# Kernel tuning notes

Hardware: AMD Instinct MI355X
Metric: run time of the kernel (lower is better)

The kernel has to match this reference:

```python
import jax, jax.numpy as jnp
import numpy as np

EPS = 1e-8  # torch cosine_similarity default eps


def compute_similarity(x, k, dilation=1):
    # x: [B, C, H, W]; returns [B, k*k-1, H, W] cosine similarity of each
    # pixel's channel vector vs its k x k neighborhood (center excluded).
    B, C, H, W = x.shape
    pad = (k // 2) * dilation
    # im2col: [B, C*k*k, H, W], channels ordered (C, kh, kw)
    patches = jax.lax.conv_general_dilated_patches(
        x, (k, k), (1, 1), padding=[(pad, pad), (pad, pad)],
        rhs_dilation=(dilation, dilation))
    patches = patches.reshape(B, C, k * k, H, W)
    center = patches[:, :, k * k // 2]                      # [B, C, H, W]
    dot = jnp.einsum('bchw,bcphw->bphw', center, patches)   # [B, k*k, H, W]
    n_center = jnp.sqrt(jnp.sum(center * center, axis=1))   # [B, H, W]
    n_patch = jnp.sqrt(jnp.sum(patches * patches, axis=1))  # [B, k*k, H, W]
    sim = dot / jnp.maximum(n_center[:, None] * n_patch, EPS)
    # drop the center (self-similarity == 1)
    c = k * k // 2
    return jnp.concatenate([sim[:, :c], sim[:, c + 1:]], axis=1)


def setup_inputs() -> dict:
    key = jax.random.key(0)
    x = jax.random.normal(key, (2, 128, 96, 96), dtype=jnp.float32)
    return {
        'x': x,
        'edge_threshold1': jnp.float32(0.3),
        'edge_threshold2': jnp.float32(0.3),
    }


def reference(x, edge_threshold1, edge_threshold2):
    LARGE_K, SMALL_K, DIL = 9, 5, 1
    large_sim = compute_similarity(x, LARGE_K, DIL)            # [B, 80, H, W]
    large_mask = (large_sim < edge_threshold1).astype(jnp.float32)
    large_mask = jnp.sqrt(jnp.sum(large_mask * large_mask, axis=1, keepdims=True))  # L2 norm over offsets
    x_mask = large_mask * x + x
    small_sim = compute_similarity(x_mask, SMALL_K, DIL)       # [B, 24, H, W]
    small_mask = (small_sim < edge_threshold2).astype(jnp.float32)
    small_mask = jnp.sqrt(jnp.sum(small_mask * small_mask, axis=1, keepdims=True))
    edge_map = x * small_mask + x
    return edge_map
```

## Files before the change

kernel.cpp:

```cpp
#include <hip/hip_runtime.h>

#define BN   2
#define CN   128
#define HN   96
#define WN   96
#define HW   (HN * WN)
#define NPIX (BN * HW)
#define NP4  (NPIX / 4)
#define NTOT (BN * CN * HW)
#define NMAP 13
#define EPSV 1e-8f

constexpr int ODY[12] = {0, 0, 1, 1, 1, 1, 1, 2, 2, 2, 2, 2};
constexpr int ODX[12] = {1, 2, -2, -1, 0, 1, 2, -2, -1, 0, 1, 2};

template<int CPC>
__global__ void __launch_bounds__(64) k_partial(const float* __restrict__ x,
                                                float* __restrict__ P) {
    int p4 = blockIdx.x * blockDim.x + threadIdx.x;
    int chunk = blockIdx.y;
    int nch = gridDim.y;
    int pix = p4 * 4;
    int b = pix / HW;
    int hw = pix - b * HW;
    int h = hw / WN;
    int w = hw - h * WN;
    const float* xb = x + ((size_t)b * CN + (size_t)chunk * CPC) * HW + h * WN + w;

    float acc[NMAP][4];
#pragma unroll
    for (int m = 0; m < NMAP; ++m)
#pragma unroll
        for (int i = 0; i < 4; ++i) acc[m][i] = 0.f;

    for (int cc = 0; cc < CPC; ++cc) {
        const float* cp = xb + (size_t)cc * HW;
        float r[3][12];
#pragma unroll
        for (int ry = 0; ry < 3; ++ry) {
            float4 a0 = make_float4(0.f, 0.f, 0.f, 0.f);
            float4 a1 = make_float4(0.f, 0.f, 0.f, 0.f);
            float4 a2 = make_float4(0.f, 0.f, 0.f, 0.f);
            if (h + ry < HN) {
                const float* rp = cp + ry * WN;
                if (w > 0)       a0 = *(const float4*)(rp - 4);
                a1 = *(const float4*)(rp);
                if (w + 4 < WN)  a2 = *(const float4*)(rp + 4);
            }
            r[ry][0] = a0.x; r[ry][1] = a0.y; r[ry][2]  = a0.z; r[ry][3]  = a0.w;
            r[ry][4] = a1.x; r[ry][5] = a1.y; r[ry][6]  = a1.z; r[ry][7]  = a1.w;
            r[ry][8] = a2.x; r[ry][9] = a2.y; r[ry][10] = a2.z; r[ry][11] = a2.w;
        }
#pragma unroll
        for (int i = 0; i < 4; ++i) {
            float c = r[0][4 + i];
            acc[0][i] += c * c;
#pragma unroll
            for (int j = 0; j < 12; ++j)
                acc[j + 1][i] += c * r[ODY[j]][4 + i + ODX[j]];
        }
    }

#pragma unroll
    for (int m = 0; m < NMAP; ++m) {
        float4 v = make_float4(acc[m][0], acc[m][1], acc[m][2], acc[m][3]);
        *(float4*)(P + ((size_t)m * nch + chunk) * NPIX + pix) = v;
    }
}

__global__ void __launch_bounds__(64) k_reduce(const float* __restrict__ P,
                                               float* __restrict__ D, int nch) {
    int t = blockIdx.x * blockDim.x + threadIdx.x;
    if (t >= NMAP * NP4) return;
    int m = t / NP4, p4 = t - m * NP4;
    int pix = p4 * 4;
    float4 s = make_float4(0.f, 0.f, 0.f, 0.f);
    for (int ch = 0; ch < nch; ++ch) {
        float4 v = *(const float4*)(P + ((size_t)m * nch + ch) * NPIX + pix);
        s.x += v.x; s.y += v.y; s.z += v.z; s.w += v.w;
    }
    *(float4*)(D + (size_t)m * NPIX + pix) = s;
}

template<int CSPLIT>
__global__ void __launch_bounds__(64) k_maskapply(const float* __restrict__ x,
                                                  const float* __restrict__ D,
                                                  const float* __restrict__ thr2p,
                                                  float* __restrict__ out) {
    int p = blockIdx.x * blockDim.x + threadIdx.x;
    if (p >= NPIX) return;
    int cg = blockIdx.y;
    const float t2 = *thr2p;
    int b = p / HW;
    int hw = p - b * HW;
    int h = hw / WN, w = hw - h * WN;

    float nc = sqrtf(D[p]);
    int count = 0;
#pragma unroll
    for (int j = 0; j < 12; ++j) {
        const int dy = ODY[j], dx = ODX[j];
        const float* Dj = D + (size_t)(j + 1) * NPIX;
        {
            float sim = 0.f;
            if (h + dy < HN && w + dx >= 0 && w + dx < WN) {
                int q = p + dy * WN + dx;
                sim = Dj[p] / fmaxf(nc * sqrtf(D[q]), EPSV);
            }
            count += (sim < t2) ? 1 : 0;
        }
        {
            float sim = 0.f;
            if (h - dy >= 0 && w - dx >= 0 && w - dx < WN) {
                int q = p - (dy * WN + dx);
                sim = Dj[q] / fmaxf(nc * sqrtf(D[q]), EPSV);
            }
            count += (sim < t2) ? 1 : 0;
        }
    }
    float s = 1.f + sqrtf((float)count);

    constexpr int CG = CN / CSPLIT;
    const float* xp = x   + ((size_t)b * CN + (size_t)cg * CG) * HW + hw;
    float*       op = out + ((size_t)b * CN + (size_t)cg * CG) * HW + hw;
#pragma unroll 8
    for (int c = 0; c < CG; ++c)
        op[(size_t)c * HW] = xp[(size_t)c * HW] * s;
}

extern "C" void kernel_launch(void* const* d_in, const int* in_sizes, int n_in,
                              void* d_out, int out_size, void* d_ws, size_t ws_size,
                              hipStream_t stream) {
    const float* x    = (const float*)d_in[0];
    const float* thr2 = (const float*)d_in[2];
    float* out = (float*)d_out;

    float* D = (float*)d_ws;
    float* P = D + (size_t)NMAP * NPIX;

    size_t base_bytes = (size_t)NMAP * NPIX * 4;
    int nch = 8;
    while (nch > 1 && base_bytes + (size_t)NMAP * nch * NPIX * 4 > ws_size) nch >>= 1;

    dim3 gA(NP4 / 64, nch);
    switch (nch) {
        case 8:  k_partial<16> <<<gA, 64, 0, stream>>>(x, P); break;
        case 4:  k_partial<32> <<<gA, 64, 0, stream>>>(x, P); break;
        case 2:  k_partial<64> <<<gA, 64, 0, stream>>>(x, P); break;
        default: k_partial<128><<<gA, 64, 0, stream>>>(x, P); break;
    }
    k_reduce<<<(NMAP * NP4 + 63) / 64, 64, 0, stream>>>(P, D, nch);
    k_maskapply<2><<<dim3(NPIX / 64, 2), 64, 0, stream>>>(x, D, thr2, out);
}
```

Before: 91.09 us.

## Fuse channel-partial and reduce kernels via in-block shared-memory tree reduction

Replaces the two-kernel scheme (per-chunk partial maps written to workspace, then a separate reduce kernel) with one kernel. Each 256-thread block covers 8 float4 pixel groups across 32 channel groups of 4 channels and reduces the 13 maps in shared memory with a tree. This removes the global-memory round trip for the partial buffers and one launch. In exchange it adds many block barriers and a large shared array that may limit occupancy. The mask-apply kernel also splits channels four ways instead of two.

```diff
diff --git a/kernel.cpp b/kernel.cpp
--- a/kernel.cpp
+++ b/kernel.cpp
@@ -7,25 +7,23 @@
 #define HW   (HN * WN)
 #define NPIX (BN * HW)
 #define NP4  (NPIX / 4)
-#define NTOT (BN * CN * HW)
 #define NMAP 13
 #define EPSV 1e-8f
 
 constexpr int ODY[12] = {0, 0, 1, 1, 1, 1, 1, 2, 2, 2, 2, 2};
 constexpr int ODX[12] = {1, 2, -2, -1, 0, 1, 2, -2, -1, 0, 1, 2};
 
-template<int CPC>
-__global__ void __launch_bounds__(64) k_partial(const float* __restrict__ x,
-                                                float* __restrict__ P) {
-    int p4 = blockIdx.x * blockDim.x + threadIdx.x;
-    int chunk = blockIdx.y;
-    int nch = gridDim.y;
+__global__ void __launch_bounds__(256) k_maps(const float* __restrict__ x,
+                                              float* __restrict__ D) {
+    const int tx = threadIdx.x;
+    const int ty = threadIdx.y;
+    int p4 = blockIdx.x * 8 + tx;
     int pix = p4 * 4;
     int b = pix / HW;
     int hw = pix - b * HW;
     int h = hw / WN;
     int w = hw - h * WN;
-    const float* xb = x + ((size_t)b * CN + (size_t)chunk * CPC) * HW + h * WN + w;
+    const float* xb = x + ((size_t)b * CN + (size_t)ty * 4) * HW + h * WN + w;
 
     float acc[NMAP][4];
 #pragma unroll
@@ -33,7 +31,8 @@
 #pragma unroll
         for (int i = 0; i < 4; ++i) acc[m][i] = 0.f;
 
-    for (int cc = 0; cc < CPC; ++cc) {
+#pragma unroll
+    for (int cc = 0; cc < 4; ++cc) {
         const float* cp = xb + (size_t)cc * HW;
         float r[3][12];
 #pragma unroll
@@ -61,25 +60,33 @@
         }
     }
 
+    __shared__ float red[16][8][53];
 #pragma unroll
-    for (int m = 0; m < NMAP; ++m) {
-        float4 v = make_float4(acc[m][0], acc[m][1], acc[m][2], acc[m][3]);
-        *(float4*)(P + ((size_t)m * nch + chunk) * NPIX + pix) = v;
+    for (int s = 16; s >= 1; s >>= 1) {
+        if (ty >= s && ty < 2 * s) {
+#pragma unroll
+            for (int m = 0; m < NMAP; ++m)
+#pragma unroll
+                for (int i = 0; i < 4; ++i)
+                    red[ty - s][tx][m * 4 + i] = acc[m][i];
+        }
+        __syncthreads();
+        if (ty < s) {
+#pragma unroll
+            for (int m = 0; m < NMAP; ++m)
+#pragma unroll
+                for (int i = 0; i < 4; ++i)
+                    acc[m][i] += red[ty][tx][m * 4 + i];
+        }
+        __syncthreads();
     }
-}
 
-__global__ void __launch_bounds__(64) k_reduce(const float* __restrict__ P,
-                                               float* __restrict__ D, int nch) {
-    int t = blockIdx.x * blockDim.x + threadIdx.x;
-    if (t >= NMAP * NP4) return;
-    int m = t / NP4, p4 = t - m * NP4;
-    int pix = p4 * 4;
-    float4 s = make_float4(0.f, 0.f, 0.f, 0.f);
-    for (int ch = 0; ch < nch; ++ch) {
-        float4 v = *(const float4*)(P + ((size_t)m * nch + ch) * NPIX + pix);
-        s.x += v.x; s.y += v.y; s.z += v.z; s.w += v.w;
+    if (ty == 0) {
+#pragma unroll
+        for (int m = 0; m < NMAP; ++m)
+            *(float4*)(D + (size_t)m * NPIX + pix) =
+                make_float4(acc[m][0], acc[m][1], acc[m][2], acc[m][3]);
     }
-    *(float4*)(D + (size_t)m * NPIX + pix) = s;
 }
 
 template<int CSPLIT>
@@ -136,19 +143,7 @@
     float* out = (float*)d_out;
 
     float* D = (float*)d_ws;
-    float* P = D + (size_t)NMAP * NPIX;
 
-    size_t base_bytes = (size_t)NMAP * NPIX * 4;
-    int nch = 8;
-    while (nch > 1 && base_bytes + (size_t)NMAP * nch * NPIX * 4 > ws_size) nch >>= 1;
-
-    dim3 gA(NP4 / 64, nch);
-    switch (nch) {
-        case 8:  k_partial<16> <<<gA, 64, 0, stream>>>(x, P); break;
-        case 4:  k_partial<32> <<<gA, 64, 0, stream>>>(x, P); break;
-        case 2:  k_partial<64> <<<gA, 64, 0, stream>>>(x, P); break;
-        default: k_partial<128><<<gA, 64, 0, stream>>>(x, P); break;
-    }
-    k_reduce<<<(NMAP * NP4 + 63) / 64, 64, 0, stream>>>(P, D, nch);
-    k_maskapply<2><<<dim3(NPIX / 64, 2), 64, 0, stream>>>(x, D, thr2, out);
+    k_maps<<<dim3(NP4 / 8), dim3(8, 32), 0, stream>>>(x, D);
+    k_maskapply<4><<<dim3(NPIX / 64, 4), 64, 0, stream>>>(x, D, thr2, out);
 }
```

Result: faster. 87.93 us (-3.5%).
